# Performance work log

Hardware: AMD Instinct MI355X
Metric: run time of the kernel (lower is better)

The kernel has to match this reference:

```python
import jax, jax.numpy as jnp
import numpy as np

BINS = 32  # position_bins


def setup_inputs() -> dict:
    key = jax.random.key(0)
    ks = jax.random.split(key, 7)
    N, IN, E = 1024, 21, 128
    return {
        "target_feat": jax.random.normal(ks[0], (N, IN), dtype=jnp.float32),
        "residue_index": jnp.arange(N, dtype=jnp.int64),
        "Wa": jax.random.normal(ks[1], (E, IN), dtype=jnp.float32) * 0.1,
        "ba": jax.random.normal(ks[2], (E,), dtype=jnp.float32) * 0.1,
        "Wb": jax.random.normal(ks[3], (E, IN), dtype=jnp.float32) * 0.1,
        "bb": jax.random.normal(ks[4], (E,), dtype=jnp.float32) * 0.1,
        "Wp": jax.random.normal(ks[5], (E, 2 * BINS + 1), dtype=jnp.float32) * 0.1,
        "bp": jax.random.normal(ks[6], (E,), dtype=jnp.float32) * 0.1,
    }


def reference(target_feat, residue_index, Wa, ba, Wb, bb, Wp, bp):
    # Linear projections: [N, E]
    a = target_feat @ Wa.T + ba
    b = target_feat @ Wb.T + bb
    # Relative position bucket: [N, N] int in [0, 2*BINS]
    d = residue_index[:, None] - residue_index[None, :]
    d = jnp.clip(d, -BINS, BINS) + BINS
    # one_hot(d) @ Wp.T + bp  ==  row gather from Wp.T (fused, no one-hot)
    p = jnp.take(Wp.T, d, axis=0) + bp  # [N, N, E]
    # Outer broadcast sum z = a_i + b_j plus position term
    return a[:, None, :] + b[None, :, :] + p
```

## Files before the change

### kernel.cpp

```cpp
#include <hip/hip_runtime.h>

#define NN   1024
#define INF  21
#define EE   128
#define NB   65
#define BINSV 32

__global__ __launch_bounds__(128) void proj_kernel(
    const float* __restrict__ tf,
    const float* __restrict__ Wa, const float* __restrict__ ba,
    const float* __restrict__ Wb, const float* __restrict__ bb,
    float* __restrict__ a, float* __restrict__ b) {
  int i = blockIdx.x;
  int e = threadIdx.x;
  __shared__ float row[INF];
  if (e < INF) row[e] = tf[i * INF + e];
  __syncthreads();
  float sa = ba[e];
  float sb = bb[e];
#pragma unroll
  for (int k = 0; k < INF; ++k) {
    float r = row[k];
    sa = fmaf(r, Wa[e * INF + k], sa);
    sb = fmaf(r, Wb[e * INF + k], sb);
  }
  a[i * EE + e] = sa;
  b[i * EE + e] = sb;
}

__global__ __launch_bounds__(128) void ptab_kernel(
    const float* __restrict__ Wp, const float* __restrict__ bp,
    float* __restrict__ ptab) {
  int d = blockIdx.x;
  int e = threadIdx.x;
  ptab[d * EE + e] = Wp[e * NB + d] + bp[e];
}

__global__ __launch_bounds__(512) void fill_kernel(
    const float* __restrict__ a, const float* __restrict__ b,
    const float* __restrict__ ptab, const int* __restrict__ ri,
    float* __restrict__ out) {
  __shared__ int sri[NN];
  for (int t = threadIdx.x; t < NN; t += 512) sri[t] = ri[t];
  __syncthreads();

  const int i  = blockIdx.x;
  const int e4 = threadIdx.x & 31;
  const int jg = threadIdx.x >> 5;

  const float4 av = reinterpret_cast<const float4*>(a + i * EE)[e4];
  const int rii = sri[i];
  float4* outrow = reinterpret_cast<float4*>(out + (size_t)i * NN * EE);

  for (int j = jg; j < NN; j += 16) {
    int d = rii - sri[j];
    d = (d < -BINSV) ? -BINSV : (d > BINSV ? BINSV : d);
    d += BINSV;
    const float4 bv = reinterpret_cast<const float4*>(b + j * EE)[e4];
    const float4 pv = reinterpret_cast<const float4*>(ptab + d * EE)[e4];
    float4 o;
    o.x = av.x + bv.x + pv.x;
    o.y = av.y + bv.y + pv.y;
    o.z = av.z + bv.z + pv.z;
    o.w = av.w + bv.w + pv.w;
    outrow[j * 32 + e4] = o;
  }
}

extern "C" void kernel_launch(void* const* d_in, const int* in_sizes, int n_in,
                              void* d_out, int out_size, void* d_ws, size_t ws_size,
                              hipStream_t stream) {
  const float* tf = (const float*)d_in[0];
  const int*   ri = (const int*)d_in[1];
  const float* Wa = (const float*)d_in[2];
  const float* ba = (const float*)d_in[3];
  const float* Wb = (const float*)d_in[4];
  const float* bb = (const float*)d_in[5];
  const float* Wp = (const float*)d_in[6];
  const float* bp = (const float*)d_in[7];
  float* out = (float*)d_out;

  float* ws   = (float*)d_ws;
  float* a    = ws;
  float* b    = ws + NN * EE;
  float* ptab = ws + 2 * NN * EE;

  proj_kernel<<<NN, 128, 0, stream>>>(tf, Wa, ba, Wb, bb, a, b);
  ptab_kernel<<<NB, 128, 0, stream>>>(Wp, bp, ptab);
  fill_kernel<<<NN, 512, 0, stream>>>(a, b, ptab, ri, out);
}
```

Measured before the change: 111.7 us.

## Fuse projections and position table into a single 2D-tiled fill kernel

Replaces the three launches (projection, position table, fill) with one kernel over 32x32 (i,j) tiles. Each block recomputes its a and b rows and the full 65x128 position table into LDS, then writes output with nontemporal stores. This removes two launches and the workspace round trip, and tiles the work. In exchange every block redoes the projection and table build redundantly and uses about 50KB of LDS, which may limit occupancy.

```diff
diff --git a/kernel.cpp b/kernel.cpp
--- a/kernel.cpp
+++ b/kernel.cpp
@@ -1,69 +1,88 @@
 #include <hip/hip_runtime.h>
 
-#define NN   1024
-#define INF  21
-#define EE   128
-#define NB   65
+#define NN    1024
+#define INF   21
+#define EE    128
+#define NB    65
 #define BINSV 32
+#define TI    32
+#define TJ    32
 
-__global__ __launch_bounds__(128) void proj_kernel(
-    const float* __restrict__ tf,
+typedef float f32x4 __attribute__((ext_vector_type(4)));
+
+__global__ __launch_bounds__(512, 4) void fused_kernel(
+    const float* __restrict__ tf, const int* __restrict__ ri,
     const float* __restrict__ Wa, const float* __restrict__ ba,
     const float* __restrict__ Wb, const float* __restrict__ bb,
-    float* __restrict__ a, float* __restrict__ b) {
-  int i = blockIdx.x;
-  int e = threadIdx.x;
-  __shared__ float row[INF];
-  if (e < INF) row[e] = tf[i * INF + e];
-  __syncthreads();
-  float sa = ba[e];
-  float sb = bb[e];
-#pragma unroll
-  for (int k = 0; k < INF; ++k) {
-    float r = row[k];
-    sa = fmaf(r, Wa[e * INF + k], sa);
-    sb = fmaf(r, Wb[e * INF + k], sb);
-  }
-  a[i * EE + e] = sa;
-  b[i * EE + e] = sb;
-}
+    const float* __restrict__ Wp, const float* __restrict__ bp,
+    float* __restrict__ out) {
+  __shared__ float a_lds[TI][EE];
+  __shared__ float b_lds[TJ][EE];
+  __shared__ float p_lds[NB][EE];
+  __shared__ float stf_i[TI][INF];
+  __shared__ float stf_j[TJ][INF];
+  __shared__ int   sri_i[TI];
+  __shared__ int   sri_j[TJ];
 
-__global__ __launch_bounds__(128) void ptab_kernel(
-    const float* __restrict__ Wp, const float* __restrict__ bp,
-    float* __restrict__ ptab) {
-  int d = blockIdx.x;
-  int e = threadIdx.x;
-  ptab[d * EE + e] = Wp[e * NB + d] + bp[e];
-}
+  const int tid = threadIdx.x;
+  const int i0 = blockIdx.y * TI;
+  const int j0 = blockIdx.x * TJ;
 
-__global__ __launch_bounds__(512) void fill_kernel(
-    const float* __restrict__ a, const float* __restrict__ b,
-    const float* __restrict__ ptab, const int* __restrict__ ri,
-    float* __restrict__ out) {
-  __shared__ int sri[NN];
-  for (int t = threadIdx.x; t < NN; t += 512) sri[t] = ri[t];
+  if (tid < TI) sri_i[tid] = ri[i0 + tid];
+  else if (tid >= 64 && tid < 64 + TJ) sri_j[tid - 64] = ri[j0 + tid - 64];
+  for (int t = tid; t < TI * INF; t += 512)
+    stf_i[t / INF][t % INF] = tf[(i0 + t / INF) * INF + (t % INF)];
+  for (int t = tid; t < TJ * INF; t += 512)
+    stf_j[t / INF][t % INF] = tf[(j0 + t / INF) * INF + (t % INF)];
   __syncthreads();
 
-  const int i  = blockIdx.x;
-  const int e4 = threadIdx.x & 31;
-  const int jg = threadIdx.x >> 5;
+  {
+    const int e  = tid & 127;
+    const int r0 = tid >> 7;
+    float wa[INF], wb[INF];
+#pragma unroll
+    for (int k = 0; k < INF; ++k) {
+      wa[k] = Wa[e * INF + k];
+      wb[k] = Wb[e * INF + k];
+    }
+    const float bav = ba[e], bbv = bb[e];
+    for (int r = r0; r < TI; r += 4) {
+      float s = bav;
+#pragma unroll
+      for (int k = 0; k < INF; ++k) s = fmaf(stf_i[r][k], wa[k], s);
+      a_lds[r][e] = s;
+    }
+    for (int r = r0; r < TJ; r += 4) {
+      float s = bbv;
+#pragma unroll
+      for (int k = 0; k < INF; ++k) s = fmaf(stf_j[r][k], wb[k], s);
+      b_lds[r][e] = s;
+    }
+    const float bpv = bp[e];
+    for (int d = r0; d < NB; d += 4)
+      p_lds[d][e] = Wp[e * NB + d] + bpv;
+  }
+  __syncthreads();
 
-  const float4 av = reinterpret_cast<const float4*>(a + i * EE)[e4];
-  const int rii = sri[i];
-  float4* outrow = reinterpret_cast<float4*>(out + (size_t)i * NN * EE);
+  const int e4 = tid & 31;
+  const int jg = tid >> 5;
+  const f32x4* __restrict__ a4 = reinterpret_cast<const f32x4*>(&a_lds[0][0]);
+  const f32x4* __restrict__ b4 = reinterpret_cast<const f32x4*>(&b_lds[0][0]);
+  const f32x4* __restrict__ p4 = reinterpret_cast<const f32x4*>(&p_lds[0][0]);
 
-  for (int j = jg; j < NN; j += 16) {
-    int d = rii - sri[j];
-    d = (d < -BINSV) ? -BINSV : (d > BINSV ? BINSV : d);
-    d += BINSV;
-    const float4 bv = reinterpret_cast<const float4*>(b + j * EE)[e4];
-    const float4 pv = reinterpret_cast<const float4*>(ptab + d * EE)[e4];
-    float4 o;
-    o.x = av.x + bv.x + pv.x;
-    o.y = av.y + bv.y + pv.y;
-    o.z = av.z + bv.z + pv.z;
-    o.w = av.w + bv.w + pv.w;
-    outrow[j * 32 + e4] = o;
+  for (int i = 0; i < TI; ++i) {
+    const f32x4 av = a4[i * 32 + e4];
+    const int rii = sri_i[i];
+    f32x4* orow = reinterpret_cast<f32x4*>(
+        out + ((size_t)(i0 + i) * NN + j0) * EE);
+#pragma unroll
+    for (int jp = 0; jp < 2; ++jp) {
+      const int j = jp * 16 + jg;
+      int d = rii - sri_j[j];
+      d = min(max(d, -BINSV), BINSV) + BINSV;
+      const f32x4 o = av + b4[j * 32 + e4] + p4[d * 32 + e4];
+      __builtin_nontemporal_store(o, orow + j * 32 + e4);
+    }
   }
 }
 
@@ -80,12 +99,6 @@
   const float* bp = (const float*)d_in[7];
   float* out = (float*)d_out;
 
-  float* ws   = (float*)d_ws;
-  float* a    = ws;
-  float* b    = ws + NN * EE;
-  float* ptab = ws + 2 * NN * EE;
-
-  proj_kernel<<<NN, 128, 0, stream>>>(tf, Wa, ba, Wb, bb, a, b);
-  ptab_kernel<<<NB, 128, 0, stream>>>(Wp, bp, ptab);
-  fill_kernel<<<NN, 512, 0, stream>>>(a, b, ptab, ri, out);
+  dim3 grid(NN / TJ, NN / TI);
+  fused_kernel<<<grid, 512, 0, stream>>>(tf, ri, Wa, ba, Wb, bb, Wp, bp, out);
 }
```

Measured after the change: 128.4 us. +15.0%, slower.
